# Kernel tuning notes

Hardware: AMD Instinct MI355X
Metric: run time of the kernel (lower is better)

## Reference

```python
import jax, jax.numpy as jnp
import numpy as np

NUM_CLASSES = 1000
FEAT_DIM = 256
N = 262144
ALPHA = 0.5


def setup_inputs() -> dict:
    key = jax.random.key(0)
    k1, k2, k3 = jax.random.split(key, 3)
    features = jax.random.normal(k1, (N, FEAT_DIM), dtype=jnp.float32)
    labels = jax.random.randint(k2, (N,), 0, NUM_CLASSES, dtype=jnp.int64)
    centers = jax.random.normal(k3, (NUM_CLASSES, FEAT_DIM), dtype=jnp.float32)
    return {"features": features, "labels": labels, "centers": centers}


def reference(features, labels, centers):
    # Fused segment-mean: scatter-add of features + per-class counts,
    # replacing the per-class python loop in the original.
    sums = jax.ops.segment_sum(features, labels, num_segments=NUM_CLASSES)  # [C, D]
    counts = jax.ops.segment_sum(
        jnp.ones((features.shape[0],), dtype=features.dtype),
        labels,
        num_segments=NUM_CLASSES,
    )  # [C]
    has_samples = counts > 0
    safe_counts = jnp.where(has_samples, counts, 1.0)
    class_means = sums / safe_counts[:, None]  # [C, D]
    # EMA update only for classes present in the batch.
    updated = (1.0 - ALPHA) * centers + ALPHA * class_means
    new_centers = jnp.where(has_samples[:, None], updated, centers)
    return new_centers
```

## Files before the change

kernel.cpp:

```cpp
#include <hip/hip_runtime.h>

constexpr int N   = 262144;
constexpr int C   = 1000;
constexpr int CP  = 1024;
constexpr int D   = 256;
constexpr int D4  = 64;
constexpr int NG  = 32;
constexpr int NSL = 16;
constexpr int NBLK = NG * NSL;
constexpr int ROWS_PER_SLICE = N / NSL;
constexpr int CLS_PER_BLK  = CP / NG;
constexpr int CLS_PER_WAVE = CLS_PER_BLK / 8;
constexpr int CAP = 96;
constexpr float ALPHA = 0.5f;

typedef float vfloat4 __attribute__((ext_vector_type(4)));


__global__ __launch_bounds__(512, 4) void accum_kernel(
        const vfloat4* __restrict__ feat4,
        const int*     __restrict__ labels,
        float*         __restrict__ partials,
        int*           __restrict__ counts_p) {
    __shared__ int lists[CLS_PER_BLK][CAP];
    __shared__ int cursor[CLS_PER_BLK];

    const int bid  = blockIdx.x;
    const int g    = bid >> 4;
    const int s    = bid & 15;
    const int tid  = threadIdx.x;
    const int w    = tid >> 6;
    const int lane = tid & 63;

    if (tid < CLS_PER_BLK) cursor[tid] = 0;
    __syncthreads();

    const int sbase = s * ROWS_PER_SLICE;
    const int4* lab4 = (const int4*)(labels + sbase);
    for (int i = tid; i < ROWS_PER_SLICE / 4; i += 512) {
        const int4 L  = lab4[i];
        const int  rb = sbase + i * 4;
        if ((L.x >> 5) == g) { int p = atomicAdd(&cursor[L.x & 31], 1); if (p < CAP) lists[L.x & 31][p] = rb + 0; }
        if ((L.y >> 5) == g) { int p = atomicAdd(&cursor[L.y & 31], 1); if (p < CAP) lists[L.y & 31][p] = rb + 1; }
        if ((L.z >> 5) == g) { int p = atomicAdd(&cursor[L.z & 31], 1); if (p < CAP) lists[L.z & 31][p] = rb + 2; }
        if ((L.w >> 5) == g) { int p = atomicAdd(&cursor[L.w & 31], 1); if (p < CAP) lists[L.w & 31][p] = rb + 3; }
    }
    __syncthreads();

    const int k0 = w * CLS_PER_WAVE;
    int cnt_[4], m_[4];
    #pragma unroll
    for (int k = 0; k < 4; ++k) {
        cnt_[k] = cursor[k0 + k];
        m_[k]   = cnt_[k] < CAP ? cnt_[k] : CAP;
    }
    int jmax = m_[0];
    #pragma unroll
    for (int k = 1; k < 4; ++k) jmax = m_[k] > jmax ? m_[k] : jmax;

    vfloat4 a0 = (vfloat4)0.f, a1 = (vfloat4)0.f,
            a2 = (vfloat4)0.f, a3 = (vfloat4)0.f;

    for (int j = 0; j < jmax; j += 2) {
        int   r[4][2];
        float wt[4][2];
        #pragma unroll
        for (int k = 0; k < 4; ++k)
            #pragma unroll
            for (int u = 0; u < 2; ++u) {
                const bool val = (j + u) < m_[k];
                r[k][u]  = val ? lists[k0 + k][j + u] : 0;
                wt[k][u] = val ? 1.f : 0.f;
            }
        vfloat4 v[4][2];
        #pragma unroll
        for (int k = 0; k < 4; ++k)
            #pragma unroll
            for (int u = 0; u < 2; ++u)
                v[k][u] = __builtin_nontemporal_load(
                              &feat4[(size_t)r[k][u] * D4 + lane]);
        #pragma unroll
        for (int u = 0; u < 2; ++u) {
            a0 += v[0][u] * wt[0][u];
            a1 += v[1][u] * wt[1][u];
            a2 += v[2][u] * wt[2][u];
            a3 += v[3][u] * wt[3][u];
        }
    }

    const vfloat4 accs[4] = {a0, a1, a2, a3};
    #pragma unroll
    for (int k = 0; k < 4; ++k) {
        const int gc = g * CLS_PER_BLK + k0 + k;
        vfloat4* outp = (vfloat4*)partials + ((size_t)s * CP + gc) * D4;
        outp[lane] = accs[k];
        if (lane == 0) counts_p[s * CP + gc] = cnt_[k];
    }
}

__global__ __launch_bounds__(256) void finalize_kernel(
        const float* __restrict__ partials,
        const int*   __restrict__ counts_p,
        const vfloat4* __restrict__ cen4,
        vfloat4*       __restrict__ out4) {
    const int c    = blockIdx.x * 4 + (threadIdx.x >> 6);
    const int lane = threadIdx.x & 63;

    vfloat4 ssum = (vfloat4)0.f;
    #pragma unroll
    for (int sl = 0; sl < NSL; ++sl)
        ssum += ((const vfloat4*)partials)[((size_t)sl * CP + c) * D4 + lane];
    int cnt = 0;
    #pragma unroll
    for (int sl = 0; sl < NSL; ++sl)
        cnt += counts_p[sl * CP + c];

    const vfloat4 cen = cen4[c * D4 + lane];
    vfloat4 o = cen;
    if (cnt > 0) o = (1.0f - ALPHA) * cen + ssum * (ALPHA / (float)cnt);
    out4[c * D4 + lane] = o;
}

extern "C" void kernel_launch(void* const* d_in, const int* in_sizes, int n_in,
                              void* d_out, int out_size, void* d_ws, size_t ws_size,
                              hipStream_t stream) {
    const vfloat4* feat4   = (const vfloat4*)d_in[0];
    const int*     labels  = (const int*)d_in[1];
    const vfloat4* cen4    = (const vfloat4*)d_in[2];
    vfloat4*       out4    = (vfloat4*)d_out;

    float* partials = (float*)d_ws;
    int*   counts_p = (int*)(partials + (size_t)NSL * CP * D);

    accum_kernel<<<NBLK, 512, 0, stream>>>(feat4, labels, partials, counts_p);
    finalize_kernel<<<C / 4, 256, 0, stream>>>(partials, counts_p, cen4, out4);
}
```

Baseline: 352.5 us.

## Flatten per-wave class lists into one packed gather list

```diff
diff --git a/kernel.cpp b/kernel.cpp
--- a/kernel.cpp
+++ b/kernel.cpp
@@ -12,6 +12,7 @@
 constexpr int CLS_PER_BLK  = CP / NG;
 constexpr int CLS_PER_WAVE = CLS_PER_BLK / 8;
 constexpr int CAP = 96;
+constexpr int FLAT_CAP = 200;
 constexpr float ALPHA = 0.5f;
 
 typedef float vfloat4 __attribute__((ext_vector_type(4)));
@@ -23,6 +24,7 @@
         float*         __restrict__ partials,
         int*           __restrict__ counts_p) {
     __shared__ int lists[CLS_PER_BLK][CAP];
+    __shared__ int flat[8][FLAT_CAP];
     __shared__ int cursor[CLS_PER_BLK];
 
     const int bid  = blockIdx.x;
@@ -48,43 +50,44 @@
     __syncthreads();
 
     const int k0 = w * CLS_PER_WAVE;
-    int cnt_[4], m_[4];
+    int cnt_[4], m_[4], base_[4];
+    int M = 0;
     #pragma unroll
     for (int k = 0; k < 4; ++k) {
-        cnt_[k] = cursor[k0 + k];
-        m_[k]   = cnt_[k] < CAP ? cnt_[k] : CAP;
+        cnt_[k]  = cursor[k0 + k];
+        m_[k]    = cnt_[k] < CAP ? cnt_[k] : CAP;
+        base_[k] = M;
+        M += m_[k];
     }
-    int jmax = m_[0];
+    if (M > FLAT_CAP) M = FLAT_CAP;
     #pragma unroll
-    for (int k = 1; k < 4; ++k) jmax = m_[k] > jmax ? m_[k] : jmax;
+    for (int k = 0; k < 4; ++k)
+        for (int idx = lane; idx < m_[k]; idx += 64)
+            if (base_[k] + idx < FLAT_CAP)
+                flat[w][base_[k] + idx] = (lists[k0 + k][idx] << 2) | k;
+    const int Mpad = (M + 7) & ~7;
+    if (lane < Mpad - M) flat[w][M + lane] = 0;
 
     vfloat4 a0 = (vfloat4)0.f, a1 = (vfloat4)0.f,
             a2 = (vfloat4)0.f, a3 = (vfloat4)0.f;
 
-    for (int j = 0; j < jmax; j += 2) {
-        int   r[4][2];
-        float wt[4][2];
+    for (int j = 0; j < Mpad; j += 8) {
+        int e[8];
         #pragma unroll
-        for (int k = 0; k < 4; ++k)
-            #pragma unroll
-            for (int u = 0; u < 2; ++u) {
-                const bool val = (j + u) < m_[k];
-                r[k][u]  = val ? lists[k0 + k][j + u] : 0;
-                wt[k][u] = val ? 1.f : 0.f;
-            }
-        vfloat4 v[4][2];
+        for (int u = 0; u < 8; ++u) e[u] = flat[w][j + u];
+        vfloat4 v[8];
         #pragma unroll
-        for (int k = 0; k < 4; ++k)
-            #pragma unroll
-            for (int u = 0; u < 2; ++u)
-                v[k][u] = __builtin_nontemporal_load(
-                              &feat4[(size_t)r[k][u] * D4 + lane]);
+        for (int u = 0; u < 8; ++u)
+            v[u] = __builtin_nontemporal_load(
+                       &feat4[(size_t)(e[u] >> 2) * D4 + lane]);
         #pragma unroll
-        for (int u = 0; u < 2; ++u) {
-            a0 += v[0][u] * wt[0][u];
-            a1 += v[1][u] * wt[1][u];
-            a2 += v[2][u] * wt[2][u];
-            a3 += v[3][u] * wt[3][u];
+        for (int u = 0; u < 8; ++u) {
+            const int  ku  = e[u] & 3;
+            const bool val = (j + u) < M;
+            a0 += v[u] * ((ku == 0 && val) ? 1.f : 0.f);
+            a1 += v[u] * ((ku == 1 && val) ? 1.f : 0.f);
+            a2 += v[u] * ((ku == 2 && val) ? 1.f : 0.f);
+            a3 += v[u] * ((ku == 3 && val) ? 1.f : 0.f);
         }
     }
 
```

Result: no change. 349.7 us (-0.8%).
